# Kernel tuning notes

Hardware: AMD Instinct MI355X
Metric: run time of the kernel (lower is better)

The kernel has to match this reference:

```python
import jax, jax.numpy as jnp
import numpy as np

B, C, H, W = 4, 64, 128, 128
NUM_HEAD = 1
SCALE = (C // NUM_HEAD) ** (-0.5)


def setup_inputs():
    key = jax.random.key(0)
    ks = jax.random.split(key, 32)
    def nrm(k, shape, s=0.05):
        return jax.random.normal(k, shape, jnp.float32) * s
    inp = {"x": jax.random.normal(ks[0], (B, C, H, W), jnp.float32)}
    i = 1
    for wn, bn in [("Wq", "bq"), ("Wk", "bk"), ("Wv", "bv"), ("Wl", "bl"), ("Wo", "bo"), ("Wp", "bp")]:
        inp[wn] = nrm(ks[i], (C, C)); i += 1
        inp[bn] = nrm(ks[i], (C,)); i += 1
    inp["sch_dw"] = nrm(ks[i], (C, 1, 5, 1)); i += 1
    inp["sch_dwb"] = nrm(ks[i], (C,)); i += 1
    inp["sch_pw"] = nrm(ks[i], (C, C, 1, 1)); i += 1
    inp["sch_pwb"] = nrm(ks[i], (C,)); i += 1
    inp["scv_dw"] = nrm(ks[i], (C, 1, 1, 5)); i += 1
    inp["scv_dwb"] = nrm(ks[i], (C,)); i += 1
    inp["scv_pw"] = nrm(ks[i], (C, C, 1, 1)); i += 1
    inp["scv_pwb"] = nrm(ks[i], (C,)); i += 1
    inp["convh_w"] = nrm(ks[i], (C, C, 1, 1)); i += 1
    inp["convh_b"] = nrm(ks[i], (C,)); i += 1
    inp["dsc_dw"] = nrm(ks[i], (C, 1, 3, 3)); i += 1
    inp["dsc_dwb"] = nrm(ks[i], (C,)); i += 1
    inp["dsc_pw"] = nrm(ks[i], (C, C, 1, 1)); i += 1
    inp["dsc_pwb"] = nrm(ks[i], (C,)); i += 1
    inp["ln_g"] = jnp.ones((C,), jnp.float32)
    inp["ln_b"] = jnp.zeros((C,), jnp.float32)
    return inp


def _linear(x, w, b):  # x [B,N,C], w [C,C] (torch Linear convention: y = x @ w.T + b)
    return x @ w.T + b


def _dwconv(x, w, b, pad):  # depthwise: x [B,C,H,W], w [C,1,kh,kw]
    y = jax.lax.conv_general_dilated(x, w, (1, 1), [(pad[0], pad[0]), (pad[1], pad[1])],
                                     dimension_numbers=("NCHW", "OIHW", "NCHW"),
                                     feature_group_count=x.shape[1])
    return y + b[None, :, None, None]


def _pwconv(x, w, b):  # 1x1 conv: w [Co,Ci,1,1]
    return jnp.einsum("bchw,oc->bohw", x, w[:, :, 0, 0]) + b[None, :, None, None]


def _attn(q, k, v):  # [B,N,C] each; dense NxN softmax attention
    a = jax.nn.softmax(jnp.einsum("bnc,bmc->bnm", q, k) * SCALE, axis=-1)
    return jnp.einsum("bnm,bmc->bnc", a, v)


def _up2_bilinear(x):  # bilinear, scale 2, align_corners=True
    Bb, Cc, Hh, Ww = x.shape
    def coords(n):
        s = jnp.linspace(0.0, n - 1.0, 2 * n)
        i0 = jnp.floor(s).astype(jnp.int32)
        i1 = jnp.minimum(i0 + 1, n - 1)
        return i0, i1, (s - i0).astype(x.dtype)
    y0, y1, wy = coords(Hh)
    x0, x1, wx = coords(Ww)
    r = x[:, :, y0, :] * (1.0 - wy)[None, None, :, None] + x[:, :, y1, :] * wy[None, None, :, None]
    return r[:, :, :, x0] * (1.0 - wx) + r[:, :, :, x1] * wx


def _forward(x, Wq, bq, Wk, bk, Wv, bv, Wl, bl, Wo, bo, Wp, bp,
             sch_dw, sch_dwb, sch_pw, sch_pwb, scv_dw, scv_dwb, scv_pw, scv_pwb,
             convh_w, convh_b, dsc_dw, dsc_dwb, dsc_pw, dsc_pwb, ln_g, ln_b):
    Bb, Cc, Hh, Ww = x.shape
    # AvgPool2d(2,2)
    xp = x.reshape(Bb, Cc, Hh // 2, 2, Ww // 2, 2).mean((3, 5))
    Hp, Wp_ = Hh // 2, Ww // 2
    N = Hp * Wp_
    # forward_lpg: GAP-gated self-attention producing low-freq prompt
    gap = xp.mean((2, 3), keepdims=True)
    xg = (gap * xp).reshape(Bb, Cc, N).transpose(0, 2, 1)  # [B,N,C]
    q = _linear(xg, Wq, bq); k = _linear(xg, Wk, bk); v = _linear(xg, Wv, bv)
    prompt_l = _linear(_attn(q, k, v), Wl, bl).transpose(0, 2, 1).reshape(Bb, Cc, Hp, Wp_)
    # forward_hpg: separable strip-conv branches -> high-freq prompt
    x_h = _pwconv(jax.nn.gelu(_dwconv(xp, sch_dw, sch_dwb, (2, 0)), approximate=False), sch_pw, sch_pwb)
    x_v = _pwconv(jax.nn.gelu(_dwconv(xp, scv_dw, scv_dwb, (0, 2)), approximate=False), scv_pw, scv_pwb)
    prompt_h = _pwconv(x_h + x_v, convh_w, convh_b)
    # forward_pgc: cross-attention Q=high, K=low, V=linear(x)
    x_V = _linear(xp.reshape(Bb, Cc, N).transpose(0, 2, 1), Wo, bo)
    x_K = prompt_l.reshape(Bb, Cc, N).transpose(0, 2, 1)
    x_Q = prompt_h.reshape(Bb, Cc, N).transpose(0, 2, 1)
    prompt = _attn(x_Q, x_K, x_V)
    prompt = _linear(prompt, Wp, bp) + x_V
    # LayerNorm over channel dim
    mu = prompt.mean(-1, keepdims=True)
    var = jnp.mean((prompt - mu) ** 2, axis=-1, keepdims=True)
    p_norm = (prompt - mu) / jnp.sqrt(var + 1e-5) * ln_g + ln_b
    p_norm = p_norm.transpose(0, 2, 1).reshape(Bb, Cc, Hp, Wp_)
    # dsc: depthwise 3x3 -> GELU -> 1x1, residual
    out = _pwconv(jax.nn.gelu(_dwconv(p_norm, dsc_dw, dsc_dwb, (1, 1)), approximate=False), dsc_pw, dsc_pwb) + p_norm
    return _up2_bilinear(out)


def reference(x, Wq, bq, Wk, bk, Wv, bv, Wl, bl, Wo, bo, Wp, bp,
              sch_dw, sch_dwb, sch_pw, sch_pwb, scv_dw, scv_dwb, scv_pw, scv_pwb,
              convh_w, convh_b, dsc_dw, dsc_dwb, dsc_pw, dsc_pwb, ln_g, ln_b):
    return _forward(x, Wq, bq, Wk, bk, Wv, bv, Wl, bl, Wo, bo, Wp, bp,
                    sch_dw, sch_dwb, sch_pw, sch_pwb, scv_dw, scv_dwb, scv_pw, scv_pwb,
                    convh_w, convh_b, dsc_dw, dsc_dwb, dsc_pw, dsc_pwb, ln_g, ln_b)
```

## Files before the change

### kernel.cpp

```cpp
#include <hip/hip_runtime.h>
#include <math.h>

#define Bn 4
#define Cn 64
#define Np 4096
#define NSPLIT 2
#define SCALE2 0.18033688011112042f

typedef unsigned short ushort_t;
typedef __attribute__((ext_vector_type(4))) float f32x4;
typedef __attribute__((ext_vector_type(8))) short bf16x8;
typedef __attribute__((ext_vector_type(4))) short bf16x4;

__device__ __forceinline__ float gelu_exact(float x) {
    return 0.5f * x * (1.0f + erff(x * 0.70710678118654752440f));
}
__device__ __forceinline__ ushort_t f2bf(float f) {
    unsigned int u = __float_as_uint(f);
    u += 0x7fffu + ((u >> 16) & 1u);
    return (ushort_t)(u >> 16);
}
__device__ __forceinline__ void gload_lds16(const ushort_t* g, ushort_t* l) {
    __builtin_amdgcn_global_load_lds(
        (const __attribute__((address_space(1))) void*)g,
        (__attribute__((address_space(3))) void*)l, 16, 0, 0);
}
__device__ __forceinline__ bf16x8 cvt8(const float v[8]) {
    bf16x8 r;
    #pragma unroll
    for (int j = 0; j < 8; ++j) r[j] = (short)f2bf(v[j]);
    return r;
}
__device__ __forceinline__ void gemm16(const bf16x8 af[2], const float* __restrict__ W,
                                       int l16, int quad, f32x4* acc) {
    #pragma unroll
    for (int cb = 0; cb < 4; ++cb) {
        #pragma unroll
        for (int ks = 0; ks < 2; ++ks) {
            const float* p = W + (cb * 16 + l16) * 64 + ks * 32 + quad * 8;
            float v[8];
            #pragma unroll
            for (int j = 0; j < 8; ++j) v[j] = p[j];
            acc[cb] = __builtin_amdgcn_mfma_f32_16x16x32_bf16(af[ks], cvt8(v), acc[cb], 0, 0, 0);
        }
    }
}
__device__ __forceinline__ void gemm16T(const bf16x8 af[2], const float* __restrict__ W,
                                        int l16, int quad, f32x4* acc) {
    #pragma unroll
    for (int cb = 0; cb < 4; ++cb) {
        #pragma unroll
        for (int ks = 0; ks < 2; ++ks) {
            const float* p = W + (cb * 16 + l16) * 64 + ks * 32 + quad * 8;
            float v[8];
            #pragma unroll
            for (int j = 0; j < 8; ++j) v[j] = p[j];
            acc[cb] = __builtin_amdgcn_mfma_f32_16x16x32_bf16(cvt8(v), af[ks], acc[cb], 0, 0, 0);
        }
    }
}
__device__ __forceinline__ void aload(const float* xs, int row, int quad, bf16x8 af[2]) {
    #pragma unroll
    for (int ks = 0; ks < 2; ++ks) {
        float v[8];
        #pragma unroll
        for (int j = 0; j < 8; ++j) v[j] = xs[(ks * 32 + quad * 8 + j) * 65 + row];
        af[ks] = cvt8(v);
    }
}
__device__ __forceinline__ void stage_bchw(const float* __restrict__ X, int b, int n0, int t,
                                           float* xs) {
    #pragma unroll
    for (int u = 0; u < 16; ++u) {
        int idx = t + u * 256;
        int c = idx >> 6, nl = idx & 63;
        xs[c * 65 + nl] = X[((size_t)(b * Cn + c)) * Np + n0 + nl];
    }
}
__device__ __forceinline__ void stage_comb(const float* __restrict__ Op, const float* linv,
                                           int b, int n0, int t, float* xs) {
    const size_t SS = (size_t)Bn * Np * Cn;
    #pragma unroll
    for (int u = 0; u < 16; ++u) {
        int idx = t + u * 256;
        int nl = idx >> 6, c = idx & 63;
        size_t gi = ((size_t)(b * Np + n0 + nl)) * Cn + c;
        xs[c * 65 + nl] = (Op[gi] + Op[SS + gi]) * linv[nl];
    }
}
__device__ __forceinline__ void store_bnc_T(ushort_t* __restrict__ Y, int b, int n, int quad,
                                            const f32x4* acc, const float* __restrict__ bias,
                                            float mult) {
    #pragma unroll
    for (int cb = 0; cb < 4; ++cb) {
        int o0 = cb * 16 + quad * 4;
        ushort4 pk;
        pk.x = f2bf((acc[cb][0] + bias[o0 + 0]) * mult);
        pk.y = f2bf((acc[cb][1] + bias[o0 + 1]) * mult);
        pk.z = f2bf((acc[cb][2] + bias[o0 + 2]) * mult);
        pk.w = f2bf((acc[cb][3] + bias[o0 + 3]) * mult);
        *(ushort4*)(Y + ((size_t)(b * Np + n)) * Cn + o0) = pk;
    }
}
__device__ __forceinline__ void store_bchw_bf16(ushort_t* __restrict__ Y, int b, int nb, int l16,
                                                const f32x4* acc, const float* __restrict__ bias) {
    #pragma unroll
    for (int cb = 0; cb < 4; ++cb) {
        int col = cb * 16 + l16;
        float bb = bias[col];
        ushort4 pk;
        pk.x = f2bf(acc[cb][0] + bb); pk.y = f2bf(acc[cb][1] + bb);
        pk.z = f2bf(acc[cb][2] + bb); pk.w = f2bf(acc[cb][3] + bb);
        *(ushort4*)(Y + ((size_t)(b * Cn + col)) * Np + nb) = pk;
    }
}

__global__ void avgpool_kernel(const float* __restrict__ x, float* __restrict__ xp,
                               float* __restrict__ gap4k,
                               const float* __restrict__ convh_w, const float* __restrict__ convh_b,
                               const float* __restrict__ sch_pw, const float* __restrict__ sch_pwb,
                               const float* __restrict__ scv_pw, const float* __restrict__ scv_pwb,
                               float* __restrict__ Wc1, float* __restrict__ Wc2,
                               float* __restrict__ bcv) {
    if (blockIdx.x < 4096) {
        int idx = blockIdx.x * 256 + threadIdx.x;
        int j  = idx & 63;
        int i  = (idx >> 6) & 63;
        int bc = idx >> 12;
        const float* p = x + ((size_t)bc * 128 + 2 * i) * 128 + 2 * j;
        float v = 0.25f * (p[0] + p[1] + p[128] + p[129]);
        xp[idx] = v;
        float s = v;
        #pragma unroll
        for (int off = 1; off < 64; off <<= 1) s += __shfl_xor(s, off, 64);
        __shared__ float sm[4];
        if ((threadIdx.x & 63) == 0) sm[threadIdx.x >> 6] = s;
        __syncthreads();
        if (threadIdx.x == 0) gap4k[blockIdx.x] = sm[0] + sm[1] + sm[2] + sm[3];
    } else {
        int g = (blockIdx.x - 4096) * 256 + threadIdx.x;
        int sel = g >> 12, idx = g & 4095;
        int o = idx >> 6, c = idx & 63;
        const float* pw = sel ? scv_pw : sch_pw;
        float acc = 0.f;
        #pragma unroll 8
        for (int m = 0; m < 64; ++m) acc += convh_w[o * 64 + m] * pw[m * 64 + c];
        (sel ? Wc2 : Wc1)[idx] = acc * SCALE2;
        if (g < 64) {
            float ab = convh_b[g];
            for (int m = 0; m < 64; ++m) ab += convh_w[g * 64 + m] * (sch_pwb[m] + scv_pwb[m]);
            bcv[g] = ab * SCALE2;
        }
    }
}

__global__ __launch_bounds__(256) void qkv_mfma(
    const float* __restrict__ xp, const float* __restrict__ gap4k,
    const float* __restrict__ Wq, const float* __restrict__ bq,
    const float* __restrict__ Wk, const float* __restrict__ bk,
    const float* __restrict__ Wv, const float* __restrict__ bv,
    const float* __restrict__ Wo, const float* __restrict__ bo,
    ushort_t* __restrict__ qb, ushort_t* __restrict__ kb, ushort_t* __restrict__ vb,
    float* __restrict__ xV, ushort_t* __restrict__ xVtb) {
    __shared__ float xs[64 * 65];
    __shared__ float gl[64];
    int b = blockIdx.y, n0 = blockIdx.x * 64, t = threadIdx.x;
    int wv_ = t >> 6, lane = t & 63, l16 = lane & 15, quad = lane >> 4;
    stage_bchw(xp, b, n0, t, xs);
    if (t < 64) {
        float s = 0.f;
        #pragma unroll
        for (int u = 0; u < 16; ++u) s += gap4k[(b * 64 + t) * 16 + u];
        gl[t] = s * (1.f / 4096.f);
    }
    __syncthreads();
    int row = wv_ * 16 + l16;
    int n   = n0 + wv_ * 16 + l16;
    int nb  = n0 + wv_ * 16 + quad * 4;
    bf16x8 ar[2], ag[2];
    #pragma unroll
    for (int ks = 0; ks < 2; ++ks) {
        float vr[8], vg[8];
        #pragma unroll
        for (int j = 0; j < 8; ++j) {
            int k = ks * 32 + quad * 8 + j;
            float xv = xs[k * 65 + row];
            vr[j] = xv; vg[j] = xv * gl[k];
        }
        ar[ks] = cvt8(vr); ag[ks] = cvt8(vg);
    }
    f32x4 acc[4];
    #pragma unroll
    for (int cb = 0; cb < 4; ++cb) acc[cb] = (f32x4){0.f, 0.f, 0.f, 0.f};
    gemm16T(ag, Wq, l16, quad, acc);
    store_bnc_T(qb, b, n, quad, acc, bq, SCALE2);
    #pragma unroll
    for (int cb = 0; cb < 4; ++cb) acc[cb] = (f32x4){0.f, 0.f, 0.f, 0.f};
    gemm16T(ag, Wk, l16, quad, acc);
    store_bnc_T(kb, b, n, quad, acc, bk, 1.f);
    #pragma unroll
    for (int cb = 0; cb < 4; ++cb) acc[cb] = (f32x4){0.f, 0.f, 0.f, 0.f};
    gemm16(ag, Wv, l16, quad, acc);
    store_bchw_bf16(vb, b, nb, l16, acc, bv);
    #pragma unroll
    for (int cb = 0; cb < 4; ++cb) acc[cb] = (f32x4){0.f, 0.f, 0.f, 0.f};
    gemm16(ar, Wo, l16, quad, acc);
    #pragma unroll
    for (int cb = 0; cb < 4; ++cb) {
        int col = cb * 16 + l16;
        float bb = bo[col];
        ushort4 pk;
        float y0 = acc[cb][0] + bb, y1 = acc[cb][1] + bb, y2 = acc[cb][2] + bb, y3 = acc[cb][3] + bb;
        xV[((size_t)(b * Np + nb + 0)) * Cn + col] = y0;
        xV[((size_t)(b * Np + nb + 1)) * Cn + col] = y1;
        xV[((size_t)(b * Np + nb + 2)) * Cn + col] = y2;
        xV[((size_t)(b * Np + nb + 3)) * Cn + col] = y3;
        pk.x = f2bf(y0); pk.y = f2bf(y1); pk.z = f2bf(y2); pk.w = f2bf(y3);
        *(ushort4*)(xVtb + ((size_t)(b * Cn + col)) * Np + nb) = pk;
    }
}

__global__ __launch_bounds__(256) void wl_mfma(
    const float* __restrict__ Op, const float* __restrict__ Lp,
    const float* __restrict__ Wl, const float* __restrict__ bl, ushort_t* __restrict__ xKb) {
    __shared__ float xs[64 * 65];
    __shared__ float linv[64];
    int b = blockIdx.y, n0 = blockIdx.x * 64, t = threadIdx.x;
    int wv_ = t >> 6, lane = t & 63, l16 = lane & 15, quad = lane >> 4;
    if (t < 64) {
        size_t li = (size_t)b * Np + n0 + t;
        linv[t] = 1.f / (Lp[li] + Lp[(size_t)Bn * Np + li]);
    }
    __syncthreads();
    stage_comb(Op, linv, b, n0, t, xs);
    __syncthreads();
    bf16x8 af[2];
    aload(xs, wv_ * 16 + l16, quad, af);
    f32x4 acc[4];
    #pragma unroll
    for (int cb = 0; cb < 4; ++cb) acc[cb] = (f32x4){0.f, 0.f, 0.f, 0.f};
    gemm16T(af, Wl, l16, quad, acc);
    store_bnc_T(xKb, b, n0 + wv_ * 16 + l16, quad, acc, bl, 1.f);
}

__global__ void dwpair_kernel(const float* __restrict__ xp,
                              const float* __restrict__ wv5, const float* __restrict__ bv5,
                              const float* __restrict__ wh5, const float* __restrict__ bh5,
                              float* __restrict__ gh, float* __restrict__ gv) {
    int idx = blockIdx.x * 256 + threadIdx.x;
    int j = idx & 63, i = (idx >> 6) & 63, bc = idx >> 12, c = bc & 63;
    const float* p = xp + (size_t)bc * Np;
    float accV = bv5[c], accH = bh5[c];
    #pragma unroll
    for (int d = 0; d < 5; ++d) {
        int ii = i + d - 2;
        if (ii >= 0 && ii < 64) accV += wv5[c * 5 + d] * p[ii * 64 + j];
        int jj = j + d - 2;
        if (jj >= 0 && jj < 64) accH += wh5[c * 5 + d] * p[i * 64 + jj];
    }
    gh[idx] = gelu_exact(accV);
    gv[idx] = gelu_exact(accH);
}

__global__ void dw3x3_gelu_kernel(const float* __restrict__ xin, const float* __restrict__ w,
                                  const float* __restrict__ bias, float* __restrict__ out) {
    int idx = blockIdx.x * 256 + threadIdx.x;
    int j = idx & 63, i = (idx >> 6) & 63, bc = idx >> 12, c = bc & 63;
    const float* p = xin + (size_t)bc * Np;
    float acc = bias[c];
    #pragma unroll
    for (int dy = 0; dy < 3; ++dy) {
        int ii = i + dy - 1;
        if (ii < 0 || ii >= 64) continue;
        #pragma unroll
        for (int dx = 0; dx < 3; ++dx) {
            int jj = j + dx - 1;
            if (jj < 0 || jj >= 64) continue;
            acc += w[c * 9 + dy * 3 + dx] * p[ii * 64 + jj];
        }
    }
    out[idx] = gelu_exact(acc);
}

__global__ __launch_bounds__(256) void hpg_mfma(
    const float* __restrict__ gh, const float* __restrict__ gv,
    const float* __restrict__ Wc1, const float* __restrict__ Wc2, const float* __restrict__ bcv,
    ushort_t* __restrict__ xQb) {
    __shared__ float xs1[64 * 65];
    __shared__ float xs2[64 * 65];
    int b = blockIdx.y, n0 = blockIdx.x * 64, t = threadIdx.x;
    int wv_ = t >> 6, lane = t & 63, l16 = lane & 15, quad = lane >> 4;
    stage_bchw(gh, b, n0, t, xs1);
    stage_bchw(gv, b, n0, t, xs2);
    __syncthreads();
    bf16x8 a1[2], a2[2];
    int row = wv_ * 16 + l16;
    aload(xs1, row, quad, a1);
    aload(xs2, row, quad, a2);
    f32x4 acc[4];
    #pragma unroll
    for (int cb = 0; cb < 4; ++cb) acc[cb] = (f32x4){0.f, 0.f, 0.f, 0.f};
    gemm16T(a1, Wc1, l16, quad, acc);
    gemm16T(a2, Wc2, l16, quad, acc);
    store_bnc_T(xQb, b, n0 + wv_ * 16 + l16, quad, acc, bcv, 1.f);
}

__global__ __launch_bounds__(256) void linln_mfma(
    const float* __restrict__ Op, const float* __restrict__ Lp,
    const float* __restrict__ Wp, const float* __restrict__ bp,
    const float* __restrict__ xV, const float* __restrict__ g, const float* __restrict__ beta,
    float* __restrict__ out) {
    __shared__ float xs[64 * 65];
    __shared__ float linv[64];
    int b = blockIdx.y, n0 = blockIdx.x * 64, t = threadIdx.x;
    int wv_ = t >> 6, lane = t & 63, l16 = lane & 15, quad = lane >> 4;
    if (t < 64) {
        size_t li = (size_t)b * Np + n0 + t;
        linv[t] = 1.f / (Lp[li] + Lp[(size_t)Bn * Np + li]);
    }
    __syncthreads();
    stage_comb(Op, linv, b, n0, t, xs);
    __syncthreads();
    bf16x8 af[2];
    aload(xs, wv_ * 16 + l16, quad, af);
    f32x4 acc[4];
    #pragma unroll
    for (int cb = 0; cb < 4; ++cb) acc[cb] = (f32x4){0.f, 0.f, 0.f, 0.f};
    gemm16(af, Wp, l16, quad, acc);
    int nb = n0 + wv_ * 16 + quad * 4;
    float vals[4][4], gc[4], bec[4];
    #pragma unroll
    for (int cb = 0; cb < 4; ++cb) {
        int col = cb * 16 + l16;
        float bb = bp[col];
        gc[cb] = g[col]; bec[cb] = beta[col];
        #pragma unroll
        for (int r = 0; r < 4; ++r)
            vals[cb][r] = acc[cb][r] + bb + xV[((size_t)(b * Np + nb + r)) * Cn + col];
    }
    f32x4 yn[4];
    #pragma unroll
    for (int r = 0; r < 4; ++r) {
        float s = 0.f, s2 = 0.f;
        #pragma unroll
        for (int cb = 0; cb < 4; ++cb) { s += vals[cb][r]; s2 += vals[cb][r] * vals[cb][r]; }
        #pragma unroll
        for (int off = 1; off < 16; off <<= 1) {
            s  += __shfl_xor(s, off, 64);
            s2 += __shfl_xor(s2, off, 64);
        }
        float mu  = s * (1.f / 64.f);
        float var = s2 * (1.f / 64.f) - mu * mu;
        float ivs = rsqrtf(var + 1e-5f);
        #pragma unroll
        for (int cb = 0; cb < 4; ++cb)
            yn[cb][r] = (vals[cb][r] - mu) * ivs * gc[cb] + bec[cb];
    }
    #pragma unroll
    for (int cb = 0; cb < 4; ++cb)
        *(f32x4*)(out + ((size_t)(b * Cn + cb * 16 + l16)) * Np + nb) = yn[cb];
}

__global__ __launch_bounds__(256) void dsc_mfma(
    const float* __restrict__ X, const float* __restrict__ W, const float* __restrict__ bias,
    const float* __restrict__ res, float* __restrict__ out) {
    __shared__ float xs[64 * 65];
    int b = blockIdx.y, n0 = blockIdx.x * 64, t = threadIdx.x;
    int wv_ = t >> 6, lane = t & 63, l16 = lane & 15, quad = lane >> 4;
    stage_bchw(X, b, n0, t, xs);
    __syncthreads();
    bf16x8 af[2];
    aload(xs, wv_ * 16 + l16, quad, af);
    f32x4 acc[4];
    #pragma unroll
    for (int cb = 0; cb < 4; ++cb) acc[cb] = (f32x4){0.f, 0.f, 0.f, 0.f};
    gemm16(af, W, l16, quad, acc);
    int nb = n0 + wv_ * 16 + quad * 4;
    #pragma unroll
    for (int cb = 0; cb < 4; ++cb) {
        int col = cb * 16 + l16;
        float bb = bias[col];
        size_t oi = ((size_t)(b * Cn + col)) * Np + nb;
        f32x4 rv = *(const f32x4*)(res + oi);
        f32x4 v4;
        #pragma unroll
        for (int r = 0; r < 4; ++r) v4[r] = acc[cb][r] + bb + rv[r];
        *(f32x4*)(out + oi) = v4;
    }
}

__global__ __launch_bounds__(128, 2) void attn_mfma_kernel(
    const ushort_t* __restrict__ Qb, const ushort_t* __restrict__ Kb,
    const ushort_t* __restrict__ Vtb, float* __restrict__ Opart, float* __restrict__ Lpart) {
    __shared__ ushort_t kt[2][64 * 64];
    __shared__ ushort_t vt[2][64 * 64];
    int b     = blockIdx.y;
    int qt    = blockIdx.x >> 1;
    int split = blockIdx.x & 1;
    int n0    = qt * 32;
    int t     = threadIdx.x;
    int wave  = t >> 6, lane = t & 63;
    int l16   = lane & 15, quad = lane >> 4;
    int sw    = l16 & 7;

    const ushort_t* qp = Qb + ((size_t)(b * Np) + n0 + wave * 16 + l16) * Cn + quad * 8;
    bf16x8 aq0 = *(const bf16x8*)(qp);
    bf16x8 aq1 = *(const bf16x8*)(qp + 32);

    f32x4 oa[4];
    float psum = 0.f;
    #pragma unroll
    for (int db = 0; db < 4; ++db) oa[db] = (f32x4){0.f, 0.f, 0.f, 0.f};

    int lrow = lane >> 3;
    int jsw  = (lane & 7) ^ (lrow & 7);
    int kvbase = split * (Np / NSPLIT);
    const ushort_t* Kg = Kb  + ((size_t)b * Np) * Cn;
    const ushort_t* Vg = Vtb + ((size_t)b * Cn) * Np;

    auto stage = [&](int buf, int k0) {
        if (wave == 0) {
            #pragma unroll
            for (int u = 0; u < 8; ++u)
                gload_lds16(Kg + ((size_t)(k0 + u * 8 + lrow)) * Cn + jsw * 8, kt[buf] + u * 512);
        } else {
            #pragma unroll
            for (int u = 0; u < 8; ++u)
                gload_lds16(Vg + ((size_t)(u * 8 + lrow)) * Np + k0 + jsw * 8, vt[buf] + u * 512);
        }
    };
    const int NT = Np / NSPLIT / 64;
    stage(0, kvbase);
    __syncthreads();

    for (int m = 0; m < NT; ++m) {
        int cur = m & 1;
        if (m + 1 < NT) stage(1 - cur, kvbase + (m + 1) * 64);
        const ushort_t* ktc = kt[cur];
        const ushort_t* vtc = vt[cur];

        f32x4 sa[4];
        #pragma unroll
        for (int cb = 0; cb < 4; ++cb) sa[cb] = (f32x4){0.f, 0.f, 0.f, 0.f};
        #pragma unroll
        for (int cb = 0; cb < 4; ++cb) {
            const ushort_t* krow = ktc + (cb * 16 + l16) * 64;
            bf16x8 bk0 = *(const bf16x8*)(krow + ((quad    ) ^ sw) * 8);
            bf16x8 bk1 = *(const bf16x8*)(krow + ((quad + 4) ^ sw) * 8);
            sa[cb] = __builtin_amdgcn_mfma_f32_16x16x32_bf16(bk0, aq0, sa[cb], 0, 0, 0);
            sa[cb] = __builtin_amdgcn_mfma_f32_16x16x32_bf16(bk1, aq1, sa[cb], 0, 0, 0);
        }
        bf16x4 pb[4];
        #pragma unroll
        for (int cb = 0; cb < 4; ++cb) {
            float p0 = exp2f(sa[cb][0]), p1 = exp2f(sa[cb][1]);
            float p2 = exp2f(sa[cb][2]), p3 = exp2f(sa[cb][3]);
            psum += (p0 + p1) + (p2 + p3);
            bf16x4 pk;
            pk[0] = (short)f2bf(p0); pk[1] = (short)f2bf(p1);
            pk[2] = (short)f2bf(p2); pk[3] = (short)f2bf(p3);
            pb[cb] = pk;
        }
        #pragma unroll
        for (int kc = 0; kc < 4; ++kc) {
            #pragma unroll
            for (int db = 0; db < 4; ++db) {
                int d = db * 16 + l16;
                const ushort_t* va = vtc + d * 64 +
                    (((kc * 2 + (quad >> 1)) ^ (d & 7)) * 8) + (quad & 1) * 4;
                bf16x4 av = *(const bf16x4*)va;
                oa[db] = __builtin_amdgcn_mfma_f32_16x16x16bf16_1k(av, pb[kc], oa[db], 0, 0, 0);
            }
        }
        __syncthreads();
    }
    psum += __shfl_xor(psum, 16, 64);
    psum += __shfl_xor(psum, 32, 64);
    size_t obase = ((size_t)(split * Bn + b)) * Np;
    int n = n0 + wave * 16 + l16;
    if (quad == 0) Lpart[obase + n] = psum;
    #pragma unroll
    for (int db = 0; db < 4; ++db)
        *(f32x4*)(Opart + (obase + n) * Cn + db * 16 + quad * 4) = oa[db];
}

__global__ void upsample_kernel(const float* __restrict__ in, float* __restrict__ out) {
    int idx = blockIdx.x * 256 + threadIdx.x;
    int x  = idx & 127;
    int y  = (idx >> 7) & 127;
    int bc = idx >> 14;
    float sy = y * (63.f / 127.f);
    float sx = x * (63.f / 127.f);
    int y0 = (int)sy, x0 = (int)sx;
    float fy = sy - y0, fx = sx - x0;
    int y1 = min(y0 + 1, 63), x1 = min(x0 + 1, 63);
    const float* p = in + (size_t)bc * Np;
    float v00 = p[y0 * 64 + x0], v01 = p[y0 * 64 + x1];
    float v10 = p[y1 * 64 + x0], v11 = p[y1 * 64 + x1];
    out[idx] = (v00 * (1.f - fx) + v01 * fx) * (1.f - fy) +
               (v10 * (1.f - fx) + v11 * fx) * fy;
}

extern "C" void kernel_launch(void* const* d_in, const int* in_sizes, int n_in,
                              void* d_out, int out_size, void* d_ws, size_t ws_size,
                              hipStream_t stream) {
    const float* x       = (const float*)d_in[0];
    const float* Wq      = (const float*)d_in[1];
    const float* bq      = (const float*)d_in[2];
    const float* Wk      = (const float*)d_in[3];
    const float* bk      = (const float*)d_in[4];
    const float* Wv      = (const float*)d_in[5];
    const float* bv      = (const float*)d_in[6];
    const float* Wl      = (const float*)d_in[7];
    const float* bl      = (const float*)d_in[8];
    const float* Wo      = (const float*)d_in[9];
    const float* bo      = (const float*)d_in[10];
    const float* Wp      = (const float*)d_in[11];
    const float* bp      = (const float*)d_in[12];
    const float* sch_dw  = (const float*)d_in[13];
    const float* sch_dwb = (const float*)d_in[14];
    const float* sch_pw  = (const float*)d_in[15];
    const float* sch_pwb = (const float*)d_in[16];
    const float* scv_dw  = (const float*)d_in[17];
    const float* scv_dwb = (const float*)d_in[18];
    const float* scv_pw  = (const float*)d_in[19];
    const float* scv_pwb = (const float*)d_in[20];
    const float* convh_w = (const float*)d_in[21];
    const float* convh_b = (const float*)d_in[22];
    const float* dsc_dw  = (const float*)d_in[23];
    const float* dsc_dwb = (const float*)d_in[24];
    const float* dsc_pw  = (const float*)d_in[25];
    const float* dsc_pwb = (const float*)d_in[26];
    const float* ln_g    = (const float*)d_in[27];
    const float* ln_b    = (const float*)d_in[28];

    float* ws = (float*)d_ws;
    const size_t SZ = (size_t)Bn * Np * Cn;
    float* xp   = ws;
    float* xV   = ws + SZ;
    float* Op   = ws + 2 * SZ;
    float* gh   = Op;
    float* gv   = Op + SZ;
    ushort_t* bws  = (ushort_t*)(ws + 4 * SZ);
    ushort_t* qb   = bws;
    ushort_t* kb_  = bws + SZ;
    ushort_t* vb   = bws + 2 * SZ;
    ushort_t* xKb  = bws + 3 * SZ;
    ushort_t* xVtb = bws + 4 * SZ;
    ushort_t* xQb  = bws + 5 * SZ;
    float* gap4k  = ws + 7 * SZ;
    float* Lpart  = gap4k + 4096;
    float* Wc1  = Lpart + (size_t)NSPLIT * Bn * Np;
    float* Wc2  = Wc1 + 4096;
    float* bcv  = Wc2 + 4096;

    dim3 g64(64, Bn);
    dim3 ga((Np / 32) * NSPLIT, Bn);

    avgpool_kernel<<<4096 + 32, 256, 0, stream>>>(x, xp, gap4k,
                                                  convh_w, convh_b, sch_pw, sch_pwb,
                                                  scv_pw, scv_pwb, Wc1, Wc2, bcv);
    qkv_mfma<<<g64, 256, 0, stream>>>(xp, gap4k, Wq, bq, Wk, bk, Wv, bv, Wo, bo,
                                      qb, kb_, vb, xV, xVtb);
    attn_mfma_kernel<<<ga, 128, 0, stream>>>(qb, kb_, vb, Op, Lpart);
    wl_mfma<<<g64, 256, 0, stream>>>(Op, Lpart, Wl, bl, xKb);
    dwpair_kernel<<<4096, 256, 0, stream>>>(xp, sch_dw, sch_dwb, scv_dw, scv_dwb, gh, gv);
    hpg_mfma<<<g64, 256, 0, stream>>>(gh, gv, Wc1, Wc2, bcv, xQb);
    attn_mfma_kernel<<<ga, 128, 0, stream>>>(xQb, xKb, xVtb, Op, Lpart);
    linln_mfma<<<g64, 256, 0, stream>>>(Op, Lpart, Wp, bp, xV, ln_g, ln_b, xp);
    dw3x3_gelu_kernel<<<4096, 256, 0, stream>>>(xp, dsc_dw, dsc_dwb, gh);
    dsc_mfma<<<g64, 256, 0, stream>>>(gh, dsc_pw, dsc_pwb, xp, gv);
    upsample_kernel<<<16384, 256, 0, stream>>>(gv, (float*)d_out);
}
```

Measured before the change: 281.2 us.

## Fuse depthwise convs into QKV and HPG into attention; split KV four ways

The separable depthwise convolution pair is folded into the QKV kernel as extra blocks that write bf16 outputs with 4-wide vectorised work. The HPG projection now runs as extra blocks inside the first attention launch, which removes two kernel launches. Attention is rewritten for 256-thread blocks with 64 queries per block and a 4-way KV split. Partial outputs are stored as bf16, and P is converted to bf16 by truncation. These changes cut the number of launches and the intermediate memory traffic, at some cost in precision and with more partial sums to combine.

```diff
diff --git a/kernel.cpp b/kernel.cpp
--- a/kernel.cpp
+++ b/kernel.cpp
@@ -4,7 +4,7 @@
 #define Bn 4
 #define Cn 64
 #define Np 4096
-#define NSPLIT 2
+#define NSPLIT 4
 #define SCALE2 0.18033688011112042f
 
 typedef unsigned short ushort_t;
@@ -19,6 +19,12 @@
     unsigned int u = __float_as_uint(f);
     u += 0x7fffu + ((u >> 16) & 1u);
     return (ushort_t)(u >> 16);
+}
+__device__ __forceinline__ ushort_t f2bf_tr(float f) {
+    return (ushort_t)(__float_as_uint(f) >> 16);
+}
+__device__ __forceinline__ float bf2f(ushort_t h) {
+    return __uint_as_float(((unsigned int)h) << 16);
 }
 __device__ __forceinline__ void gload_lds16(const ushort_t* g, ushort_t* l) {
     __builtin_amdgcn_global_load_lds(
@@ -77,7 +83,7 @@
         xs[c * 65 + nl] = X[((size_t)(b * Cn + c)) * Np + n0 + nl];
     }
 }
-__device__ __forceinline__ void stage_comb(const float* __restrict__ Op, const float* linv,
+__device__ __forceinline__ void stage_comb(const ushort_t* __restrict__ OpB, const float* linv,
                                            int b, int n0, int t, float* xs) {
     const size_t SS = (size_t)Bn * Np * Cn;
     #pragma unroll
@@ -85,7 +91,9 @@
         int idx = t + u * 256;
         int nl = idx >> 6, c = idx & 63;
         size_t gi = ((size_t)(b * Np + n0 + nl)) * Cn + c;
-        xs[c * 65 + nl] = (Op[gi] + Op[SS + gi]) * linv[nl];
+        float s = bf2f(OpB[gi]) + bf2f(OpB[SS + gi]) +
+                  bf2f(OpB[2 * SS + gi]) + bf2f(OpB[3 * SS + gi]);
+        xs[c * 65 + nl] = s * linv[nl];
     }
 }
 __device__ __forceinline__ void store_bnc_T(ushort_t* __restrict__ Y, int b, int n, int quad,
@@ -154,17 +162,55 @@
     }
 }
 
-__global__ __launch_bounds__(256) void qkv_mfma(
+__global__ __launch_bounds__(256) void qkv_dw_kernel(
     const float* __restrict__ xp, const float* __restrict__ gap4k,
     const float* __restrict__ Wq, const float* __restrict__ bq,
     const float* __restrict__ Wk, const float* __restrict__ bk,
     const float* __restrict__ Wv, const float* __restrict__ bv,
     const float* __restrict__ Wo, const float* __restrict__ bo,
     ushort_t* __restrict__ qb, ushort_t* __restrict__ kb, ushort_t* __restrict__ vb,
-    float* __restrict__ xV, ushort_t* __restrict__ xVtb) {
+    float* __restrict__ xV, ushort_t* __restrict__ xVtb,
+    const float* __restrict__ wv5, const float* __restrict__ bv5,
+    const float* __restrict__ wh5, const float* __restrict__ bh5,
+    ushort_t* __restrict__ gh, ushort_t* __restrict__ gv) {
+    int b = blockIdx.y, t = threadIdx.x;
+    if (blockIdx.x >= 64) {
+        int part = blockIdx.x - 64;
+        int e = part * 1024 + t * 4;
+        size_t base = (size_t)b * (Cn * Np) + e;
+        int c = e >> 12, i = (e >> 6) & 63, j = e & 63;
+        const float* p = xp + ((size_t)(b * Cn + c)) * Np;
+        float accV[4], accH[4];
+        #pragma unroll
+        for (int k = 0; k < 4; ++k) { accV[k] = bv5[c]; accH[k] = bh5[c]; }
+        #pragma unroll
+        for (int d = 0; d < 5; ++d) {
+            int ii = i + d - 2;
+            if (ii >= 0 && ii < 64) {
+                #pragma unroll
+                for (int k = 0; k < 4; ++k) accV[k] += wv5[c * 5 + d] * p[ii * 64 + j + k];
+            }
+        }
+        #pragma unroll
+        for (int k = 0; k < 4; ++k) {
+            #pragma unroll
+            for (int d = 0; d < 5; ++d) {
+                int jj = j + k + d - 2;
+                if (jj >= 0 && jj < 64) accH[k] += wh5[c * 5 + d] * p[i * 64 + jj];
+            }
+        }
+        ushort4 ph, pv_;
+        ph.x = f2bf(gelu_exact(accV[0])); ph.y = f2bf(gelu_exact(accV[1]));
+        ph.z = f2bf(gelu_exact(accV[2])); ph.w = f2bf(gelu_exact(accV[3]));
+        pv_.x = f2bf(gelu_exact(accH[0])); pv_.y = f2bf(gelu_exact(accH[1]));
+        pv_.z = f2bf(gelu_exact(accH[2])); pv_.w = f2bf(gelu_exact(accH[3]));
+        *(ushort4*)(gh + base) = ph;
+        *(ushort4*)(gv + base) = pv_;
+        return;
+    }
     __shared__ float xs[64 * 65];
     __shared__ float gl[64];
-    int b = blockIdx.y, n0 = blockIdx.x * 64, t = threadIdx.x;
+    int n0 = blockIdx.x * 64;
     int wv_ = t >> 6, lane = t & 63, l16 = lane & 15, quad = lane >> 4;
     stage_bchw(xp, b, n0, t, xs);
     if (t < 64) {
@@ -220,8 +266,166 @@
     }
 }
 
+__device__ __forceinline__ void attn_body(
+    int xblk, int b, const ushort_t* __restrict__ Qb, const ushort_t* __restrict__ Kb,
+    const ushort_t* __restrict__ Vtb, ushort_t* __restrict__ OpB, float* __restrict__ Lpart,
+    ushort_t* smem) {
+    ushort_t* kt0 = smem;
+    ushort_t* vt0 = smem + 8192;
+    int split = xblk >> 6;
+    int qt    = xblk & 63;
+    int n0    = qt * 64;
+    int t     = threadIdx.x;
+    int wave  = t >> 6, lane = t & 63;
+    int l16   = lane & 15, quad = lane >> 4;
+
+    const ushort_t* qp = Qb + ((size_t)(b * Np) + n0 + wave * 16 + l16) * Cn + quad * 8;
+    bf16x8 aq0 = *(const bf16x8*)(qp);
+    bf16x8 aq1 = *(const bf16x8*)(qp + 32);
+
+    f32x4 oa[4];
+    float psum = 0.f;
+    #pragma unroll
+    for (int db = 0; db < 4; ++db) oa[db] = (f32x4){0.f, 0.f, 0.f, 0.f};
+
+    int lrow = lane >> 3;
+    int kvbase = split * (Np / NSPLIT);
+    const ushort_t* Kg = Qb == nullptr ? nullptr : Kb + ((size_t)b * Np) * Cn;
+    const ushort_t* Vg = Vtb + ((size_t)b * Cn) * Np;
+
+    auto stage = [&](int buf, int k0) {
+        int wh = wave & 1;
+        if (wave < 2) {
+            ushort_t* dst = kt0 + buf * 4096 + wh * 2048;
+            #pragma unroll
+            for (int u = 0; u < 4; ++u) {
+                int r = wh * 32 + u * 8 + lrow;
+                int jsw = ((lane & 7) ^ lrow ^ (wh * 4 + u)) & 7;
+                gload_lds16(Kg + ((size_t)(k0 + r)) * Cn + jsw * 8, dst + u * 512);
+            }
+        } else {
+            ushort_t* dst = vt0 + buf * 4096 + wh * 2048;
+            #pragma unroll
+            for (int u = 0; u < 4; ++u) {
+                int d = wh * 32 + u * 8 + lrow;
+                int jsw = ((lane & 7) ^ lrow ^ (wh * 4 + u)) & 7;
+                gload_lds16(Vg + (size_t)d * Np + k0 + jsw * 8, dst + u * 512);
+            }
+        }
+    };
+    const int NT = (Np / NSPLIT) / 64;
+    stage(0, kvbase);
+    __syncthreads();
+
+    for (int m = 0; m < NT; ++m) {
+        int cur = m & 1;
+        if (m + 1 < NT) stage(1 - cur, kvbase + (m + 1) * 64);
+        const ushort_t* ktc = kt0 + cur * 4096;
+        const ushort_t* vtc = vt0 + cur * 4096;
+
+        f32x4 sa[4];
+        #pragma unroll
+        for (int cb = 0; cb < 4; ++cb) sa[cb] = (f32x4){0.f, 0.f, 0.f, 0.f};
+        #pragma unroll
+        for (int cb = 0; cb < 4; ++cb) {
+            int key = ((l16 & 7) ^ (cb * 2 + (l16 >> 3))) & 7;
+            const ushort_t* krow = ktc + (cb * 16 + l16) * 64;
+            bf16x8 bk0 = *(const bf16x8*)(krow + ((quad    ) ^ key) * 8);
+            bf16x8 bk1 = *(const bf16x8*)(krow + ((quad + 4) ^ key) * 8);
+            sa[cb] = __builtin_amdgcn_mfma_f32_16x16x32_bf16(bk0, aq0, sa[cb], 0, 0, 0);
+            sa[cb] = __builtin_amdgcn_mfma_f32_16x16x32_bf16(bk1, aq1, sa[cb], 0, 0, 0);
+        }
+        bf16x4 pb[4];
+        #pragma unroll
+        for (int cb = 0; cb < 4; ++cb) {
+            float p0 = exp2f(sa[cb][0]), p1 = exp2f(sa[cb][1]);
+            float p2 = exp2f(sa[cb][2]), p3 = exp2f(sa[cb][3]);
+            psum += (p0 + p1) + (p2 + p3);
+            bf16x4 pk;
+            pk[0] = (short)f2bf_tr(p0); pk[1] = (short)f2bf_tr(p1);
+            pk[2] = (short)f2bf_tr(p2); pk[3] = (short)f2bf_tr(p3);
+            pb[cb] = pk;
+        }
+        #pragma unroll
+        for (int kc = 0; kc < 4; ++kc) {
+            #pragma unroll
+            for (int db = 0; db < 4; ++db) {
+                int d = db * 16 + l16;
+                int key = ((l16 & 7) ^ (db * 2 + (l16 >> 3))) & 7;
+                int phys = (kc * 2 + (quad >> 1)) ^ key;
+                const ushort_t* va = vtc + d * 64 + phys * 8 + (quad & 1) * 4;
+                bf16x4 av = *(const bf16x4*)va;
+                oa[db] = __builtin_amdgcn_mfma_f32_16x16x16bf16_1k(av, pb[kc], oa[db], 0, 0, 0);
+            }
+        }
+        __syncthreads();
+    }
+    psum += __shfl_xor(psum, 16, 64);
+    psum += __shfl_xor(psum, 32, 64);
+    size_t obase = ((size_t)(split * Bn + b)) * Np;
+    int n = n0 + wave * 16 + l16;
+    if (quad == 0) Lpart[obase + n] = psum;
+    #pragma unroll
+    for (int db = 0; db < 4; ++db) {
+        ushort4 pk;
+        pk.x = f2bf(oa[db][0]); pk.y = f2bf(oa[db][1]);
+        pk.z = f2bf(oa[db][2]); pk.w = f2bf(oa[db][3]);
+        *(ushort4*)(OpB + (obase + n) * Cn + db * 16 + quad * 4) = pk;
+    }
+}
+
+__device__ __forceinline__ void hpg_body(
+    int tile, int b, const ushort_t* __restrict__ gh, const ushort_t* __restrict__ gv,
+    const float* __restrict__ Wc1, const float* __restrict__ Wc2, const float* __restrict__ bcv,
+    ushort_t* __restrict__ xQb, ushort_t* smem) {
+    ushort_t* xs1 = smem;
+    ushort_t* xs2 = smem + 4608;
+    int n0 = tile * 64, t = threadIdx.x;
+    int wv_ = t >> 6, lane = t & 63, l16 = lane & 15, quad = lane >> 4;
+    #pragma unroll
+    for (int u = 0; u < 4; ++u) {
+        int lin = u * 256 + t;
+        int c = lin >> 4, nl4 = (lin & 15) * 4;
+        size_t gi = ((size_t)(b * Cn + c)) * Np + n0 + nl4;
+        ushort4 g1 = *(const ushort4*)(gh + gi);
+        ushort4 g2 = *(const ushort4*)(gv + gi);
+        xs1[(nl4 + 0) * 72 + c] = g1.x; xs1[(nl4 + 1) * 72 + c] = g1.y;
+        xs1[(nl4 + 2) * 72 + c] = g1.z; xs1[(nl4 + 3) * 72 + c] = g1.w;
+        xs2[(nl4 + 0) * 72 + c] = g2.x; xs2[(nl4 + 1) * 72 + c] = g2.y;
+        xs2[(nl4 + 2) * 72 + c] = g2.z; xs2[(nl4 + 3) * 72 + c] = g2.w;
+    }
+    __syncthreads();
+    int row = wv_ * 16 + l16;
+    bf16x8 a1[2], a2[2];
+    #pragma unroll
+    for (int ks = 0; ks < 2; ++ks) {
+        a1[ks] = *(const bf16x8*)(xs1 + row * 72 + ks * 32 + quad * 8);
+        a2[ks] = *(const bf16x8*)(xs2 + row * 72 + ks * 32 + quad * 8);
+    }
+    f32x4 acc[4];
+    #pragma unroll
+    for (int cb = 0; cb < 4; ++cb) acc[cb] = (f32x4){0.f, 0.f, 0.f, 0.f};
+    gemm16T(a1, Wc1, l16, quad, acc);
+    gemm16T(a2, Wc2, l16, quad, acc);
+    store_bnc_T(xQb, b, n0 + wv_ * 16 + l16, quad, acc, bcv, 1.f);
+}
+
+__global__ __launch_bounds__(256) void attn_hpg_kernel(
+    const ushort_t* __restrict__ Qb, const ushort_t* __restrict__ Kb,
+    const ushort_t* __restrict__ Vtb, ushort_t* __restrict__ OpB, float* __restrict__ Lpart,
+    const ushort_t* __restrict__ gh, const ushort_t* __restrict__ gv,
+    const float* __restrict__ Wc1, const float* __restrict__ Wc2,
+    const float* __restrict__ bcv, ushort_t* __restrict__ xQb) {
+    __shared__ ushort_t smem[16384];
+    int b = blockIdx.y;
+    if (blockIdx.x < 256)
+        attn_body(blockIdx.x, b, Qb, Kb, Vtb, OpB, Lpart, smem);
+    else
+        hpg_body(blockIdx.x - 256, b, gh, gv, Wc1, Wc2, bcv, xQb, smem);
+}
+
 __global__ __launch_bounds__(256) void wl_mfma(
-    const float* __restrict__ Op, const float* __restrict__ Lp,
+    const ushort_t* __restrict__ OpB, const float* __restrict__ Lp,
     const float* __restrict__ Wl, const float* __restrict__ bl, ushort_t* __restrict__ xKb) {
     __shared__ float xs[64 * 65];
     __shared__ float linv[64];
@@ -229,10 +433,11 @@
     int wv_ = t >> 6, lane = t & 63, l16 = lane & 15, quad = lane >> 4;
     if (t < 64) {
         size_t li = (size_t)b * Np + n0 + t;
-        linv[t] = 1.f / (Lp[li] + Lp[(size_t)Bn * Np + li]);
-    }
-    __syncthreads();
-    stage_comb(Op, linv, b, n0, t, xs);
+        const size_t LS = (size_t)Bn * Np;
+        linv[t] = 1.f / (Lp[li] + Lp[LS + li] + Lp[2 * LS + li] + Lp[3 * LS + li]);
+    }
+    __syncthreads();
+    stage_comb(OpB, linv, b, n0, t, xs);
     __syncthreads();
     bf16x8 af[2];
     aload(xs, wv_ * 16 + l16, quad, af);
@@ -243,70 +448,8 @@
     store_bnc_T(xKb, b, n0 + wv_ * 16 + l16, quad, acc, bl, 1.f);
 }
 
-__global__ void dwpair_kernel(const float* __restrict__ xp,
-                              const float* __restrict__ wv5, const float* __restrict__ bv5,
-                              const float* __restrict__ wh5, const float* __restrict__ bh5,
-                              float* __restrict__ gh, float* __restrict__ gv) {
-    int idx = blockIdx.x * 256 + threadIdx.x;
-    int j = idx & 63, i = (idx >> 6) & 63, bc = idx >> 12, c = bc & 63;
-    const float* p = xp + (size_t)bc * Np;
-    float accV = bv5[c], accH = bh5[c];
-    #pragma unroll
-    for (int d = 0; d < 5; ++d) {
-        int ii = i + d - 2;
-        if (ii >= 0 && ii < 64) accV += wv5[c * 5 + d] * p[ii * 64 + j];
-        int jj = j + d - 2;
-        if (jj >= 0 && jj < 64) accH += wh5[c * 5 + d] * p[i * 64 + jj];
-    }
-    gh[idx] = gelu_exact(accV);
-    gv[idx] = gelu_exact(accH);
-}
-
-__global__ void dw3x3_gelu_kernel(const float* __restrict__ xin, const float* __restrict__ w,
-                                  const float* __restrict__ bias, float* __restrict__ out) {
-    int idx = blockIdx.x * 256 + threadIdx.x;
-    int j = idx & 63, i = (idx >> 6) & 63, bc = idx >> 12, c = bc & 63;
-    const float* p = xin + (size_t)bc * Np;
-    float acc = bias[c];
-    #pragma unroll
-    for (int dy = 0; dy < 3; ++dy) {
-        int ii = i + dy - 1;
-        if (ii < 0 || ii >= 64) continue;
-        #pragma unroll
-        for (int dx = 0; dx < 3; ++dx) {
-            int jj = j + dx - 1;
-            if (jj < 0 || jj >= 64) continue;
-            acc += w[c * 9 + dy * 3 + dx] * p[ii * 64 + jj];
-        }
-    }
-    out[idx] = gelu_exact(acc);
-}
-
-__global__ __launch_bounds__(256) void hpg_mfma(
-    const float* __restrict__ gh, const float* __restrict__ gv,
-    const float* __restrict__ Wc1, const float* __restrict__ Wc2, const float* __restrict__ bcv,
-    ushort_t* __restrict__ xQb) {
-    __shared__ float xs1[64 * 65];
-    __shared__ float xs2[64 * 65];
-    int b = blockIdx.y, n0 = blockIdx.x * 64, t = threadIdx.x;
-    int wv_ = t >> 6, lane = t & 63, l16 = lane & 15, quad = lane >> 4;
-    stage_bchw(gh, b, n0, t, xs1);
-    stage_bchw(gv, b, n0, t, xs2);
-    __syncthreads();
-    bf16x8 a1[2], a2[2];
-    int row = wv_ * 16 + l16;
-    aload(xs1, row, quad, a1);
-    aload(xs2, row, quad, a2);
-    f32x4 acc[4];
-    #pragma unroll
-    for (int cb = 0; cb < 4; ++cb) acc[cb] = (f32x4){0.f, 0.f, 0.f, 0.f};
-    gemm16T(a1, Wc1, l16, quad, acc);
-    gemm16T(a2, Wc2, l16, quad, acc);
-    store_bnc_T(xQb, b, n0 + wv_ * 16 + l16, quad, acc, bcv, 1.f);
-}
-
 __global__ __launch_bounds__(256) void linln_mfma(
-    const float* __restrict__ Op, const float* __restrict__ Lp,
+    const ushort_t* __restrict__ OpB, const float* __restrict__ Lp,
     const float* __restrict__ Wp, const float* __restrict__ bp,
     const float* __restrict__ xV, const float* __restrict__ g, const float* __restrict__ beta,
     float* __restrict__ out) {
@@ -316,10 +459,11 @@
     int wv_ = t >> 6, lane = t & 63, l16 = lane & 15, quad = lane >> 4;
     if (t < 64) {
         size_t li = (size_t)b * Np + n0 + t;
-        linv[t] = 1.f / (Lp[li] + Lp[(size_t)Bn * Np + li]);
-    }
-    __syncthreads();
-    stage_comb(Op, linv, b, n0, t, xs);
+        const size_t LS = (size_t)Bn * Np;
+        linv[t] = 1.f / (Lp[li] + Lp[LS + li] + Lp[2 * LS + li] + Lp[3 * LS + li]);
+    }
+    __syncthreads();
+    stage_comb(OpB, linv, b, n0, t, xs);
     __syncthreads();
     bf16x8 af[2];
     aload(xs, wv_ * 16 + l16, quad, af);
@@ -359,6 +503,26 @@
     #pragma unroll
     for (int cb = 0; cb < 4; ++cb)
         *(f32x4*)(out + ((size_t)(b * Cn + cb * 16 + l16)) * Np + nb) = yn[cb];
+}
+
+__global__ void dw3x3_gelu_kernel(const float* __restrict__ xin, const float* __restrict__ w,
+                                  const float* __restrict__ bias, float* __restrict__ out) {
+    int idx = blockIdx.x * 256 + threadIdx.x;
+    int j = idx & 63, i = (idx >> 6) & 63, bc = idx >> 12, c = bc & 63;
+    const float* p = xin + (size_t)bc * Np;
+    float acc = bias[c];
+    #pragma unroll
+    for (int dy = 0; dy < 3; ++dy) {
+        int ii = i + dy - 1;
+        if (ii < 0 || ii >= 64) continue;
+        #pragma unroll
+        for (int dx = 0; dx < 3; ++dx) {
+            int jj = j + dx - 1;
+            if (jj < 0 || jj >= 64) continue;
+            acc += w[c * 9 + dy * 3 + dx] * p[ii * 64 + jj];
+        }
+    }
+    out[idx] = gelu_exact(acc);
 }
 
 __global__ __launch_bounds__(256) void dsc_mfma(
@@ -387,101 +551,6 @@
         for (int r = 0; r < 4; ++r) v4[r] = acc[cb][r] + bb + rv[r];
         *(f32x4*)(out + oi) = v4;
     }
-}
-
-__global__ __launch_bounds__(128, 2) void attn_mfma_kernel(
-    const ushort_t* __restrict__ Qb, const ushort_t* __restrict__ Kb,
-    const ushort_t* __restrict__ Vtb, float* __restrict__ Opart, float* __restrict__ Lpart) {
-    __shared__ ushort_t kt[2][64 * 64];
-    __shared__ ushort_t vt[2][64 * 64];
-    int b     = blockIdx.y;
-    int qt    = blockIdx.x >> 1;
-    int split = blockIdx.x & 1;
-    int n0    = qt * 32;
-    int t     = threadIdx.x;
-    int wave  = t >> 6, lane = t & 63;
-    int l16   = lane & 15, quad = lane >> 4;
-    int sw    = l16 & 7;
-
-    const ushort_t* qp = Qb + ((size_t)(b * Np) + n0 + wave * 16 + l16) * Cn + quad * 8;
-    bf16x8 aq0 = *(const bf16x8*)(qp);
-    bf16x8 aq1 = *(const bf16x8*)(qp + 32);
-
-    f32x4 oa[4];
-    float psum = 0.f;
-    #pragma unroll
-    for (int db = 0; db < 4; ++db) oa[db] = (f32x4){0.f, 0.f, 0.f, 0.f};
-
-    int lrow = lane >> 3;
-    int jsw  = (lane & 7) ^ (lrow & 7);
-    int kvbase = split * (Np / NSPLIT);
-    const ushort_t* Kg = Kb  + ((size_t)b * Np) * Cn;
-    const ushort_t* Vg = Vtb + ((size_t)b * Cn) * Np;
-
-    auto stage = [&](int buf, int k0) {
-        if (wave == 0) {
-            #pragma unroll
-            for (int u = 0; u < 8; ++u)
-                gload_lds16(Kg + ((size_t)(k0 + u * 8 + lrow)) * Cn + jsw * 8, kt[buf] + u * 512);
-        } else {
-            #pragma unroll
-            for (int u = 0; u < 8; ++u)
-                gload_lds16(Vg + ((size_t)(u * 8 + lrow)) * Np + k0 + jsw * 8, vt[buf] + u * 512);
-        }
-    };
-    const int NT = Np / NSPLIT / 64;
-    stage(0, kvbase);
-    __syncthreads();
-
-    for (int m = 0; m < NT; ++m) {
-        int cur = m & 1;
-        if (m + 1 < NT) stage(1 - cur, kvbase + (m + 1) * 64);
-        const ushort_t* ktc = kt[cur];
-        const ushort_t* vtc = vt[cur];
-
-        f32x4 sa[4];
-        #pragma unroll
-        for (int cb = 0; cb < 4; ++cb) sa[cb] = (f32x4){0.f, 0.f, 0.f, 0.f};
-        #pragma unroll
-        for (int cb = 0; cb < 4; ++cb) {
-            const ushort_t* krow = ktc + (cb * 16 + l16) * 64;
-            bf16x8 bk0 = *(const bf16x8*)(krow + ((quad    ) ^ sw) * 8);
-            bf16x8 bk1 = *(const bf16x8*)(krow + ((quad + 4) ^ sw) * 8);
-            sa[cb] = __builtin_amdgcn_mfma_f32_16x16x32_bf16(bk0, aq0, sa[cb], 0, 0, 0);
-            sa[cb] = __builtin_amdgcn_mfma_f32_16x16x32_bf16(bk1, aq1, sa[cb], 0, 0, 0);
-        }
-        bf16x4 pb[4];
-        #pragma unroll
-        for (int cb = 0; cb < 4; ++cb) {
-            float p0 = exp2f(sa[cb][0]), p1 = exp2f(sa[cb][1]);
-            float p2 = exp2f(sa[cb][2]), p3 = exp2f(sa[cb][3]);
-            psum += (p0 + p1) + (p2 + p3);
-            bf16x4 pk;
-            pk[0] = (short)f2bf(p0); pk[1] = (short)f2bf(p1);
-            pk[2] = (short)f2bf(p2); pk[3] = (short)f2bf(p3);
-            pb[cb] = pk;
-        }
-        #pragma unroll
-        for (int kc = 0; kc < 4; ++kc) {
-            #pragma unroll
-            for (int db = 0; db < 4; ++db) {
-                int d = db * 16 + l16;
-                const ushort_t* va = vtc + d * 64 +
-                    (((kc * 2 + (quad >> 1)) ^ (d & 7)) * 8) + (quad & 1) * 4;
-                bf16x4 av = *(const bf16x4*)va;
-                oa[db] = __builtin_amdgcn_mfma_f32_16x16x16bf16_1k(av, pb[kc], oa[db], 0, 0, 0);
-            }
-        }
-        __syncthreads();
-    }
-    psum += __shfl_xor(psum, 16, 64);
-    psum += __shfl_xor(psum, 32, 64);
-    size_t obase = ((size_t)(split * Bn + b)) * Np;
-    int n = n0 + wave * 16 + l16;
-    if (quad == 0) Lpart[obase + n] = psum;
-    #pragma unroll
-    for (int db = 0; db < 4; ++db)
-        *(f32x4*)(Opart + (obase + n) * Cn + db * 16 + quad * 4) = oa[db];
 }
 
 __global__ void upsample_kernel(const float* __restrict__ in, float* __restrict__ out) {
@@ -538,37 +607,39 @@
     const size_t SZ = (size_t)Bn * Np * Cn;
     float* xp   = ws;
     float* xV   = ws + SZ;
-    float* Op   = ws + 2 * SZ;
-    float* gh   = Op;
-    float* gv   = Op + SZ;
-    ushort_t* bws  = (ushort_t*)(ws + 4 * SZ);
+    ushort_t* ghb = (ushort_t*)(ws + 2 * SZ);
+    ushort_t* gh  = ghb;
+    ushort_t* gv  = ghb + SZ;
+    float* f2   = ws + 2 * SZ;
+    ushort_t* bws  = (ushort_t*)(ws + 3 * SZ);
     ushort_t* qb   = bws;
     ushort_t* kb_  = bws + SZ;
     ushort_t* vb   = bws + 2 * SZ;
     ushort_t* xKb  = bws + 3 * SZ;
     ushort_t* xVtb = bws + 4 * SZ;
     ushort_t* xQb  = bws + 5 * SZ;
-    float* gap4k  = ws + 7 * SZ;
+    ushort_t* OpB  = (ushort_t*)(ws + 6 * SZ);
+    float* gap4k  = ws + 8 * SZ;
     float* Lpart  = gap4k + 4096;
     float* Wc1  = Lpart + (size_t)NSPLIT * Bn * Np;
     float* Wc2  = Wc1 + 4096;
     float* bcv  = Wc2 + 4096;
 
     dim3 g64(64, Bn);
-    dim3 ga((Np / 32) * NSPLIT, Bn);
 
     avgpool_kernel<<<4096 + 32, 256, 0, stream>>>(x, xp, gap4k,
                                                   convh_w, convh_b, sch_pw, sch_pwb,
                                                   scv_pw, scv_pwb, Wc1, Wc2, bcv);
-    qkv_mfma<<<g64, 256, 0, stream>>>(xp, gap4k, Wq, bq, Wk, bk, Wv, bv, Wo, bo,
-                                      qb, kb_, vb, xV, xVtb);
-    attn_mfma_kernel<<<ga, 128, 0, stream>>>(qb, kb_, vb, Op, Lpart);
-    wl_mfma<<<g64, 256, 0, stream>>>(Op, Lpart, Wl, bl, xKb);
-    dwpair_kernel<<<4096, 256, 0, stream>>>(xp, sch_dw, sch_dwb, scv_dw, scv_dwb, gh, gv);
-    hpg_mfma<<<g64, 256, 0, stream>>>(gh, gv, Wc1, Wc2, bcv, xQb);
-    attn_mfma_kernel<<<ga, 128, 0, stream>>>(xQb, xKb, xVtb, Op, Lpart);
-    linln_mfma<<<g64, 256, 0, stream>>>(Op, Lpart, Wp, bp, xV, ln_g, ln_b, xp);
-    dw3x3_gelu_kernel<<<4096, 256, 0, stream>>>(xp, dsc_dw, dsc_dwb, gh);
-    dsc_mfma<<<g64, 256, 0, stream>>>(gh, dsc_pw, dsc_pwb, xp, gv);
-    upsample_kernel<<<16384, 256, 0, stream>>>(gv, (float*)d_out);
-}
+    qkv_dw_kernel<<<dim3(64 + 256, Bn), 256, 0, stream>>>(
+        xp, gap4k, Wq, bq, Wk, bk, Wv, bv, Wo, bo,
+        qb, kb_, vb, xV, xVtb, sch_dw, sch_dwb, scv_dw, scv_dwb, gh, gv);
+    attn_hpg_kernel<<<dim3(256 + 64, Bn), 256, 0, stream>>>(
+        qb, kb_, vb, OpB, Lpart, gh, gv, Wc1, Wc2, bcv, xQb);
+    wl_mfma<<<g64, 256, 0, stream>>>(OpB, Lpart, Wl, bl, xKb);
+    attn_hpg_kernel<<<dim3(256, Bn), 256, 0, stream>>>(
+        xQb, xKb, xVtb, OpB, Lpart, gh, gv, Wc1, Wc2, bcv, xQb);
+    linln_mfma<<<g64, 256, 0, stream>>>(OpB, Lpart, Wp, bp, xV, ln_g, ln_b, xp);
+    dw3x3_gelu_kernel<<<4096, 256, 0, stream>>>(xp, dsc_dw, dsc_dwb, xV);
+    dsc_mfma<<<g64, 256, 0, stream>>>(xV, dsc_pw, dsc_pwb, xp, f2);
+    upsample_kernel<<<16384, 256, 0, stream>>>(f2, (float*)d_out);
+}
```

After: 243.9 us. -13.3%, faster.
